# Kernel tuning notes

Hardware: AMD Instinct MI355X
Metric: run time of the kernel (lower is better)

## Reference

```python
import jax, jax.numpy as jnp
import numpy as np

N_NODES = 100000
N_EDGES = 1600000
C = 256            # in_channels == out_channels
NUM_BUNDLES = 64
BUNDLE_DIM = 2
NUM_GRAPHS = 128
BN_EPS = 1e-5


def setup_inputs() -> dict:
    key = jax.random.key(0)
    ks = jax.random.split(key, 12)
    x = jax.random.normal(ks[0], (N_NODES, C), dtype=jnp.float32)
    edge_index = jax.random.randint(ks[1], (2, N_EDGES), 0, N_NODES, dtype=jnp.int64)
    batch = jnp.sort(jax.random.randint(ks[2], (N_NODES,), 0, NUM_GRAPHS, dtype=jnp.int64))
    s = 0.05
    # struct_enc MLP: Linear(C, 2*NB) -> GELU -> Linear(2*NB, NB)
    se_w1 = jax.random.normal(ks[3], (C, 2 * NUM_BUNDLES), dtype=jnp.float32) * s
    se_b1 = jnp.zeros((2 * NUM_BUNDLES,), dtype=jnp.float32)
    se_w2 = jax.random.normal(ks[4], (2 * NUM_BUNDLES, NUM_BUNDLES), dtype=jnp.float32) * s
    se_b2 = jnp.zeros((NUM_BUNDLES,), dtype=jnp.float32)
    # LimConv.lin: Linear(C, C)
    lin_w = jax.random.normal(ks[5], (C, C), dtype=jnp.float32) * s
    lin_b = jnp.zeros((C,), dtype=jnp.float32)
    # BatchNorm1d affine params
    bn_gamma = jnp.ones((C,), dtype=jnp.float32)
    bn_beta = jnp.zeros((C,), dtype=jnp.float32)
    return {"x": x, "edge_index": edge_index, "batch": batch,
            "se_w1": se_w1, "se_b1": se_b1, "se_w2": se_w2, "se_b2": se_b2,
            "lin_w": lin_w, "lin_b": lin_b, "bn_gamma": bn_gamma, "bn_beta": bn_beta}


def _lim_layer(x, batch, se_w1, se_b1, se_w2, se_b2, lin_w, lin_b, bn_gamma, bn_beta):
    n = x.shape[0]
    # vector field: [N, NB, 2, fiber]
    vf = x.reshape(n, NUM_BUNDLES, BUNDLE_DIM, -1)
    # struct_enc MLP -> per-bundle angle (tanh-squashed), euler map to SO(2)
    h1 = jax.nn.gelu(x @ se_w1 + se_b1, approximate=False)
    ang = jnp.tanh(h1 @ se_w2 + se_b2)          # [N, NB]
    c, s = jnp.cos(ang), jnp.sin(ang)
    # R[n,b] = [[c,-s],[s,c]]  -> [N, NB, 2, 2]
    rot = jnp.stack([jnp.stack([c, -s], axis=-1),
                     jnp.stack([s, c], axis=-1)], axis=-2)
    # rotate fibers
    vf = jnp.einsum('nbij,nbjf->nbif', rot, vf)
    h = vf.reshape(n, C) @ lin_w + lin_b
    # global mean pool over graphs, then broadcast back to nodes
    sums = jax.ops.segment_sum(h, batch, num_segments=NUM_GRAPHS)
    cnts = jax.ops.segment_sum(jnp.ones((n,), h.dtype), batch, num_segments=NUM_GRAPHS)
    hmean = sums / jnp.maximum(cnts, 1.0)[:, None]
    h = hmean[batch]
    # inverse rotation (R^T)
    vf = h.reshape(n, NUM_BUNDLES, BUNDLE_DIM, -1)
    vf = jnp.einsum('nbji,nbjf->nbif', rot, vf)
    h = vf.reshape(n, C)
    # residual (dim_in == dim_out)
    h = x + h
    # dropout p=0 / eval -> identity. BatchNorm1d with batch statistics.
    mu = jnp.mean(h, axis=0)
    var = jnp.var(h, axis=0)
    h = (h - mu) * jax.lax.rsqrt(var + BN_EPS) * bn_gamma + bn_beta
    return h


def reference(x, edge_index, batch, se_w1, se_b1, se_w2, se_b2, lin_w, lin_b, bn_gamma, bn_beta):
    # edge_index is unused when num_gnn == 0 (struct_enc is an MLP), as in the source.
    del edge_index
    return _lim_layer(x, batch, se_w1, se_b1, se_w2, se_b2, lin_w, lin_b, bn_gamma, bn_beta)
```

## Files before the change

### kernel.cpp

```cpp
#include <hip/hip_runtime.h>
#include <hip/hip_bf16.h>
#include <math.h>

#define N_NODES 100000
#define C 256
#define NB 64
#define H1D 128
#define NG 128
#define BN_EPS 1e-5f

#define BLKN 32
#define ROWS 64
#define SUBT 2
#define NBLK1 ((N_NODES + ROWS - 1) / ROWS)
#define NPART NBLK1

#define GREC 769

#define OFF_GSUMS 0
#define OFF_BNSUM (NG * GREC)
#define OFF_BNSQ  (OFF_BNSUM + 256)
#define ZERO_FLOATS (OFF_BNSQ + 256)
#define OFF_HMEAN ZERO_FLOATS
#define OFF_WT1   (OFF_HMEAN + NG * C)
#define OFF_WT2   (OFF_WT1 + 16896)
#define OFF_CSN   (OFF_WT2 + 4352)
#define OFF_PBN   (OFF_CSN + N_NODES * 64)

#define WT1_LD 264
#define WT2_LD 136
#define XS_LD  272

typedef __attribute__((ext_vector_type(8))) short bf16x8;
typedef __attribute__((ext_vector_type(4))) float f32x4;

struct __align__(8) bf4 { __hip_bfloat16 x, y, z, w; };

__device__ __forceinline__ float bf2f(__hip_bfloat16 h) { return __bfloat162float(h); }

__device__ __forceinline__ float fast_tanh(float y) {
    float e = __expf(2.f * y);
    return 1.f - 2.f / (e + 1.f);
}
__device__ __forceinline__ float fast_gelu(float v) {
    float u = 0.7978845608f * (v + 0.044715f * v * v * v);
    return 0.5f * v * (1.f + fast_tanh(u));
}

__global__ __launch_bounds__(256)
void k0_prep(const float* __restrict__ W1, const float* __restrict__ W2,
             __hip_bfloat16* __restrict__ Wt1, __hip_bfloat16* __restrict__ Wt2)
{
    const int t0 = threadIdx.x + blockIdx.x * 256;
    const int stride = gridDim.x * 256;
    for (int i = t0; i < 128 * 256; i += stride) {
        int n = i >> 8, k = i & 255;
        Wt1[n * WT1_LD + k] = __float2bfloat16(W1[k * 128 + n]);
    }
    for (int i = t0; i < 64 * 128; i += stride) {
        int n = i >> 7, k = i & 127;
        Wt2[n * WT2_LD + k] = __float2bfloat16(W2[k * 64 + n]);
    }
}

__global__ __launch_bounds__(256, 6)
void k1_angles_rot_pool(const float* __restrict__ x,
                        const int* __restrict__ batch,
                        const __hip_bfloat16* __restrict__ Wt1g,
                        const float* __restrict__ b1,
                        const __hip_bfloat16* __restrict__ Wt2g,
                        const float* __restrict__ b2,
                        float* __restrict__ gsums,
                        float* __restrict__ pbn,
                        __hip_bfloat16* __restrict__ csng)
{
    __shared__ __hip_bfloat16 xs[BLKN][XS_LD];
    __shared__ char sm_u[BLKN * WT2_LD * 2];
    __shared__ int gsh[BLKN];
    auto h1s = (__hip_bfloat16 (*)[WT2_LD])sm_u;
    auto csn = (__hip_bfloat16 (*)[132])sm_u;

    const int t = threadIdx.x;
    const int w = t >> 6;
    const int l = t & 63;
    const int lo = l & 15, quad = l >> 4;

    const short* w1base = (const short*)Wt1g + (w * 32 + lo) * WT1_LD + quad * 8;
    const int mw = w >> 1;
    const int nb0 = (w & 1) * 32;
    const short* w2base = (const short*)Wt2g + (nb0 + lo) * WT2_LD + quad * 8;
    const float bb1_0 = b1[w * 32 + lo];
    const float bb1_1 = b1[w * 32 + 16 + lo];
    const float bb2_0 = b2[nb0 + lo];
    const float bb2_1 = b2[nb0 + 16 + lo];

    const int pr = t >> 6;
    const int pc4 = (t & 63) * 4;

    const int c = t;
    const int b = c >> 2;
    const int idx2 = c & 3;
    float xc_a = 0.f, xs_a = 0.f, st = 0.f, rcnt = 0.f;
    float xm = 0.f, xq = 0.f;
    int gprev = -1;

#define FLUSH_G(gidx) do {                               \
        float* rec = gsums + (size_t)(gidx) * GREC;      \
        atomicAdd(&rec[c], xc_a);                        \
        atomicAdd(&rec[256 + c], xs_a);                  \
        atomicAdd(&rec[512 + c], st);                    \
        if (c == 0) atomicAdd(&rec[768], rcnt);          \
    } while (0)

    float4 pf[8];
    int pb = 0;
    {
        const int n0 = blockIdx.x * ROWS;
        #pragma unroll
        for (int m = 0; m < 8; ++m)
            pf[m] = *(const float4*)(x + (size_t)(n0 + pr + m * 4) * C + pc4);
        if (t < BLKN) pb = batch[n0 + t];
    }

    for (int sub = 0; sub < SUBT; ++sub) {
        const int n0 = blockIdx.x * ROWS + sub * BLKN;
        if (n0 >= N_NODES) break;

        #pragma unroll
        for (int m = 0; m < 8; ++m) {
            bf4 pk;
            pk.x = __float2bfloat16(pf[m].x); pk.y = __float2bfloat16(pf[m].y);
            pk.z = __float2bfloat16(pf[m].z); pk.w = __float2bfloat16(pf[m].w);
            *(bf4*)&xs[pr + m * 4][pc4] = pk;
        }
        if (t < BLKN) gsh[t] = pb;

        const int n1 = n0 + BLKN;
        const bool more = (sub + 1 < SUBT) && (n1 < N_NODES);
        if (more) {
            #pragma unroll
            for (int m = 0; m < 8; ++m)
                pf[m] = *(const float4*)(x + (size_t)(n1 + pr + m * 4) * C + pc4);
            if (t < BLKN) pb = batch[n1 + t];
        }
        __syncthreads();

        f32x4 acc1[2][2];
        #pragma unroll
        for (int mt = 0; mt < 2; ++mt) { acc1[mt][0] = (f32x4)0.f; acc1[mt][1] = (f32x4)0.f; }
        #pragma unroll
        for (int k = 0; k < 8; ++k) {
            bf16x8 bA = *(const bf16x8*)(w1base + k * 32);
            bf16x8 bB = *(const bf16x8*)(w1base + 16 * WT1_LD + k * 32);
            #pragma unroll
            for (int mt = 0; mt < 2; ++mt) {
                bf16x8 afr = *(const bf16x8*)&xs[mt * 16 + lo][k * 32 + quad * 8];
                acc1[mt][0] = __builtin_amdgcn_mfma_f32_16x16x32_bf16(afr, bA, acc1[mt][0], 0, 0, 0);
                acc1[mt][1] = __builtin_amdgcn_mfma_f32_16x16x32_bf16(afr, bB, acc1[mt][1], 0, 0, 0);
            }
        }
        #pragma unroll
        for (int nt = 0; nt < 2; ++nt) {
            const float bb = nt ? bb1_1 : bb1_0;
            #pragma unroll
            for (int mt = 0; mt < 2; ++mt) {
                #pragma unroll
                for (int r = 0; r < 4; ++r) {
                    float v = fast_gelu(acc1[mt][nt][r] + bb);
                    h1s[mt * 16 + quad * 4 + r][w * 32 + nt * 16 + lo] = __float2bfloat16(v);
                }
            }
        }
        __syncthreads();

        f32x4 acc2[2];
        acc2[0] = (f32x4)0.f; acc2[1] = (f32x4)0.f;
        #pragma unroll
        for (int k = 0; k < 4; ++k) {
            bf16x8 afr = *(const bf16x8*)&h1s[mw * 16 + lo][k * 32 + quad * 8];
            bf16x8 bA = *(const bf16x8*)(w2base + k * 32);
            bf16x8 bB = *(const bf16x8*)(w2base + 16 * WT2_LD + k * 32);
            acc2[0] = __builtin_amdgcn_mfma_f32_16x16x32_bf16(afr, bA, acc2[0], 0, 0, 0);
            acc2[1] = __builtin_amdgcn_mfma_f32_16x16x32_bf16(afr, bB, acc2[1], 0, 0, 0);
        }
        __syncthreads();

        #pragma unroll
        for (int nt = 0; nt < 2; ++nt) {
            const int col = nb0 + nt * 16 + lo;
            const float bb = nt ? bb2_1 : bb2_0;
            #pragma unroll
            for (int r = 0; r < 4; ++r) {
                float a = fast_tanh(acc2[nt][r] + bb);
                union { unsigned int u; __hip_bfloat16 h[2]; } p;
                p.h[0] = __float2bfloat16(__cosf(a));
                p.h[1] = __float2bfloat16(__sinf(a));
                *(unsigned int*)&csn[mw * 16 + quad * 4 + r][2 * col] = p.u;
            }
        }
        __syncthreads();

        #pragma unroll
        for (int m = 0; m < 4; ++m) {
            int idx = t + m * 256;
            int row = idx >> 5;
            int q = (idx & 31);
            uint2 v = *(const uint2*)&csn[row][q * 4];
            *(uint2*)(csng + (size_t)(n0 + row) * 128 + q * 4) = v;
        }

        #pragma unroll 8
        for (int r = 0; r < BLKN; ++r) {
            const int g = gsh[r];
            if (g != gprev) {
                if (gprev >= 0) FLUSH_G(gprev);
                xc_a = 0.f; xs_a = 0.f; st = 0.f; rcnt = 0.f;
                gprev = g;
            }
            const float xv = bf2f(xs[r][c]);
            union { unsigned int u; __hip_bfloat16 h[2]; } cs;
            cs.u = *(const unsigned int*)&csn[r][2 * b];
            const float cv = bf2f(cs.h[0]);
            const float sv = bf2f(cs.h[1]);
            xc_a += xv * cv;
            xs_a += xv * sv;
            xm += xv;
            xq += xv * xv;
            st += (idx2 == 0) ? cv : (idx2 == 1) ? sv : (idx2 == 2) ? cv * cv : cv * sv;
            rcnt += 1.f;
        }
        __syncthreads();
    }

    if (gprev >= 0) FLUSH_G(gprev);
    pbn[(size_t)blockIdx.x * 512 + t] = xm;
    pbn[(size_t)blockIdx.x * 512 + 256 + t] = xq;
#undef FLUSH_G
}

__global__ __launch_bounds__(256)
void k2_hmean_stats(const float* __restrict__ gsums,
                    const float* __restrict__ pbn,
                    const float* __restrict__ lin_w, const float* __restrict__ lin_b,
                    float* __restrict__ hmean,
                    float* __restrict__ bnsum, float* __restrict__ bnsq)
{
    __shared__ float xc[C], xsv[C], bs4[C], grot[C], hm[C];
    __shared__ float cnt_sh;
    const int g = blockIdx.x;
    const int t = threadIdx.x;

    {
        const int chunk = (NPART + NG - 1) / NG;
        const int r0 = g * chunk;
        const int r1 = (r0 + chunk < NPART) ? (r0 + chunk) : NPART;
        if (r0 < r1) {
            float a0 = 0.f, a1 = 0.f;
            for (int r = r0; r < r1; ++r) {
                a0 += pbn[(size_t)r * 512 + t];
                a1 += pbn[(size_t)r * 512 + 256 + t];
            }
            atomicAdd(&bnsum[t], a0);
            atomicAdd(&bnsq[t], a1);
        }
    }

    const float* rec = gsums + (size_t)g * GREC;
    xc[t]  = rec[t];
    xsv[t] = rec[256 + t];
    bs4[t] = rec[512 + t];
    if (t == 0) cnt_sh = rec[768];
    __syncthreads();

    const int b = t >> 2, idx2 = t & 3, i2 = idx2 >> 1;
    grot[t] = (i2 == 0) ? (xc[t] - xsv[t + 2]) : (xsv[t - 2] + xc[t]);
    __syncthreads();

    float a0 = 0.f, a1 = 0.f, a2 = 0.f, a3 = 0.f;
    #pragma unroll 4
    for (int k = 0; k < C; k += 4) {
        a0 += grot[k + 0] * lin_w[(size_t)(k + 0) * C + t];
        a1 += grot[k + 1] * lin_w[(size_t)(k + 1) * C + t];
        a2 += grot[k + 2] * lin_w[(size_t)(k + 2) * C + t];
        a3 += grot[k + 3] * lin_w[(size_t)(k + 3) * C + t];
    }
    const float cnt = cnt_sh;
    const float hv = (cnt > 0.f) ? ((a0 + a1 + a2 + a3) / cnt + lin_b[t]) : 0.f;
    hm[t] = hv;
    hmean[g * C + t] = hv;
    __syncthreads();

    if (cnt > 0.f) {
        const int f = idx2 & 1;
        const float h0 = hm[4 * b + f];
        const float h1 = hm[4 * b + 2 + f];
        const float CV = bs4[4 * b + 0], SV = bs4[4 * b + 1];
        const float CC = bs4[4 * b + 2], CS = bs4[4 * b + 3];
        const float SS = cnt - CC;
        float sumc, sqc;
        if (i2 == 0) {
            sumc = h0 * CV + h1 * SV;
            sqc  = 2.f * (h0 * xc[t] + h1 * xsv[t])
                 + h0 * h0 * CC + 2.f * h0 * h1 * CS + h1 * h1 * SS;
        } else {
            sumc = -h0 * SV + h1 * CV;
            sqc  = 2.f * (-h0 * xsv[t] + h1 * xc[t])
                 + h0 * h0 * SS - 2.f * h0 * h1 * CS + h1 * h1 * CC;
        }
        atomicAdd(&bnsum[t], sumc);
        atomicAdd(&bnsq[t], sqc);
    }
}

__global__ __launch_bounds__(256, 4)
void k4_fused(const float* __restrict__ x,
              const int* __restrict__ batch,
              const __hip_bfloat16* __restrict__ csng,
              const float* __restrict__ hmean,
              const float* __restrict__ bnsum, const float* __restrict__ bnsq,
              const float* __restrict__ gamma, const float* __restrict__ beta,
              float* __restrict__ out)
{
    __shared__ float mul_s[C], add_s[C];
    const int t = threadIdx.x;
    {
        const float inv_n = 1.0f / (float)N_NODES;
        const float mu = bnsum[t] * inv_n;
        const float var = bnsq[t] * inv_n - mu * mu;
        const float inv = rsqrtf(var + BN_EPS);
        const float m = gamma[t] * inv;
        mul_s[t] = m;
        add_s[t] = beta[t] - mu * m;
    }
    __syncthreads();
    const int s = t >> 6;
    const int cg = t & 63;
    const float4 mm = *(const float4*)&mul_s[cg * 4];
    const float4 aa = *(const float4*)&add_s[cg * 4];

    for (int base = blockIdx.x * 4; base < N_NODES; base += gridDim.x * 4) {
        const int n = base + s;
        if (n < N_NODES) {
            const int g = batch[n];
            const float4 hm = *(const float4*)(hmean + (size_t)g * C + cg * 4);
            union { unsigned int u; __hip_bfloat16 h[2]; } cs;
            cs.u = *(const unsigned int*)(csng + (size_t)n * 128 + cg * 2);
            const float cv = bf2f(cs.h[0]);
            const float sv = bf2f(cs.h[1]);
            const float4 xv = *(const float4*)(x + (size_t)n * C + cg * 4);
            float4 o;
            o.x = (xv.x + cv * hm.x + sv * hm.z) * mm.x + aa.x;
            o.y = (xv.y + cv * hm.y + sv * hm.w) * mm.y + aa.y;
            o.z = (xv.z - sv * hm.x + cv * hm.z) * mm.z + aa.z;
            o.w = (xv.w - sv * hm.y + cv * hm.w) * mm.w + aa.w;
            *(float4*)(out + (size_t)n * C + cg * 4) = o;
        }
    }
}

extern "C" void kernel_launch(void* const* d_in, const int* in_sizes, int n_in,
                              void* d_out, int out_size, void* d_ws, size_t ws_size,
                              hipStream_t stream)
{
    const float* x      = (const float*)d_in[0];
    const int* batch    = (const int*)d_in[2];
    const float* W1     = (const float*)d_in[3];
    const float* b1     = (const float*)d_in[4];
    const float* W2     = (const float*)d_in[5];
    const float* b2     = (const float*)d_in[6];
    const float* lin_w  = (const float*)d_in[7];
    const float* lin_b  = (const float*)d_in[8];
    const float* gamma  = (const float*)d_in[9];
    const float* beta   = (const float*)d_in[10];

    float* ws    = (float*)d_ws;
    float* gsums = ws + OFF_GSUMS;
    float* bnsum = ws + OFF_BNSUM;
    float* bnsq  = ws + OFF_BNSQ;
    float* hmean = ws + OFF_HMEAN;
    __hip_bfloat16* Wt1  = (__hip_bfloat16*)(ws + OFF_WT1);
    __hip_bfloat16* Wt2  = (__hip_bfloat16*)(ws + OFF_WT2);
    __hip_bfloat16* csng = (__hip_bfloat16*)(ws + OFF_CSN);
    float* pbn   = ws + OFF_PBN;
    float* out   = (float*)d_out;

    hipMemsetAsync(gsums, 0, ZERO_FLOATS * sizeof(float), stream);

    k0_prep<<<32, 256, 0, stream>>>(W1, W2, Wt1, Wt2);
    k1_angles_rot_pool<<<NBLK1, 256, 0, stream>>>(x, batch, Wt1, b1, Wt2, b2,
                                                  gsums, pbn, csng);
    k2_hmean_stats<<<NG, 256, 0, stream>>>(gsums, pbn, lin_w, lin_b, hmean, bnsum, bnsq);
    k4_fused<<<2048, 256, 0, stream>>>(x, batch, csng, hmean, bnsum, bnsq,
                                       gamma, beta, out);
}
```

Measured before the change: 297.4 us.

## Fuse all stages into one persistent cooperative kernel with grid syncs

Replaces the memset plus four separate launches with a single cooperative persistent kernel. Grid-wide syncs separate the weight prep and zeroing, the angle/rotation/pool pass, the per-graph hmean and BN stats, and the final normalize pass. Each block now processes a contiguous range of 32-row subtiles, which reduces per-block partials and atomic flushes. The aim is to remove launch gaps and tail effects. In exchange it caps the grid at about 1024 resident blocks, adds grid-sync overhead, and keeps the old path as a fallback.

New measurement: 607.8 us. 2.04x slower.

```diff
diff --git a/kernel.cpp b/kernel.cpp
--- a/kernel.cpp
+++ b/kernel.cpp
@@ -1,6 +1,9 @@
 #include <hip/hip_runtime.h>
+#include <hip/hip_cooperative_groups.h>
 #include <hip/hip_bf16.h>
 #include <math.h>
+
+namespace cg = cooperative_groups;
 
 #define N_NODES 100000
 #define C 256
@@ -10,10 +13,13 @@
 #define BN_EPS 1e-5f
 
 #define BLKN 32
-#define ROWS 64
-#define SUBT 2
-#define NBLK1 ((N_NODES + ROWS - 1) / ROWS)
-#define NPART NBLK1
+#define NSUB (N_NODES / BLKN)
+#define COOP_MAX 1024
+
+#define FB_ROWS 64
+#define FB_SUBT 2
+#define FB_NBLK ((N_NODES + FB_ROWS - 1) / FB_ROWS)
+#define PBN_ROWS FB_NBLK
 
 #define GREC 769
 
@@ -45,6 +51,325 @@
 __device__ __forceinline__ float fast_gelu(float v) {
     float u = 0.7978845608f * (v + 0.044715f * v * v * v);
     return 0.5f * v * (1.f + fast_tanh(u));
+}
+
+__global__ __launch_bounds__(256, 4)
+void fused(const float* __restrict__ x,
+           const int* __restrict__ batch,
+           const float* __restrict__ W1, const float* __restrict__ b1,
+           const float* __restrict__ W2, const float* __restrict__ b2,
+           const float* __restrict__ lin_w, const float* __restrict__ lin_b,
+           const float* __restrict__ gamma, const float* __restrict__ beta,
+           float* __restrict__ ws, float* __restrict__ out)
+{
+    __shared__ __hip_bfloat16 xs[BLKN][XS_LD];
+    __shared__ char sm_u[BLKN * WT2_LD * 2];
+    __shared__ int gsh[BLKN];
+    auto h1s = (__hip_bfloat16 (*)[WT2_LD])sm_u;
+    auto csn = (__hip_bfloat16 (*)[132])sm_u;
+
+    float* gsums = ws + OFF_GSUMS;
+    float* bnsum = ws + OFF_BNSUM;
+    float* bnsq  = ws + OFF_BNSQ;
+    float* hmean = ws + OFF_HMEAN;
+    __hip_bfloat16* Wt1g = (__hip_bfloat16*)(ws + OFF_WT1);
+    __hip_bfloat16* Wt2g = (__hip_bfloat16*)(ws + OFF_WT2);
+    __hip_bfloat16* csng = (__hip_bfloat16*)(ws + OFF_CSN);
+    float* pbn   = ws + OFF_PBN;
+
+    cg::grid_group gg = cg::this_grid();
+
+    const int nblk = gridDim.x;
+    const int bid = blockIdx.x;
+    const int t = threadIdx.x;
+    const int w = t >> 6;
+    const int l = t & 63;
+    const int lo = l & 15, quad = l >> 4;
+
+    {
+        for (int i = bid * 256 + t; i < ZERO_FLOATS; i += nblk * 256)
+            ws[i] = 0.f;
+        if (bid < 32) {
+            const int t0 = bid * 256 + t;
+            for (int j = t0; j < 128 * 256; j += 8192) {
+                int nn = j >> 8, k = j & 255;
+                Wt1g[nn * WT1_LD + k] = __float2bfloat16(W1[k * 128 + nn]);
+            }
+            for (int j = t0; j < 64 * 128; j += 8192) {
+                int nn = j >> 7, k = j & 127;
+                Wt2g[nn * WT2_LD + k] = __float2bfloat16(W2[k * 64 + nn]);
+            }
+        }
+    }
+    __threadfence();
+    gg.sync();
+
+    {
+        const int base_cnt = NSUB / nblk;
+        const int rem = NSUB - base_cnt * nblk;
+        const int scnt = base_cnt + (bid < rem ? 1 : 0);
+        const int sstart = base_cnt * bid + (bid < rem ? bid : rem);
+
+        const short* w1base = (const short*)Wt1g + (w * 32 + lo) * WT1_LD + quad * 8;
+        const int mw = w >> 1;
+        const int nb0 = (w & 1) * 32;
+        const short* w2base = (const short*)Wt2g + (nb0 + lo) * WT2_LD + quad * 8;
+        const float bb1_0 = b1[w * 32 + lo];
+        const float bb1_1 = b1[w * 32 + 16 + lo];
+        const float bb2_0 = b2[nb0 + lo];
+        const float bb2_1 = b2[nb0 + 16 + lo];
+
+        const int pr = t >> 6;
+        const int pc4 = (t & 63) * 4;
+
+        const int c = t;
+        const int b = c >> 2;
+        const int idx2 = c & 3;
+        float xc_a = 0.f, xs_a = 0.f, st = 0.f, rcnt = 0.f;
+        float xm = 0.f, xq = 0.f;
+        int gprev = -1;
+
+#define FLUSH_G(gidx) do {                               \
+        float* rec = gsums + (size_t)(gidx) * GREC;      \
+        atomicAdd(&rec[c], xc_a);                        \
+        atomicAdd(&rec[256 + c], xs_a);                  \
+        atomicAdd(&rec[512 + c], st);                    \
+        if (c == 0) atomicAdd(&rec[768], rcnt);          \
+    } while (0)
+
+        float4 pf[8];
+        int pb = 0;
+        {
+            const int n0 = sstart * BLKN;
+            #pragma unroll
+            for (int m = 0; m < 8; ++m)
+                pf[m] = *(const float4*)(x + (size_t)(n0 + pr + m * 4) * C + pc4);
+            if (t < BLKN) pb = batch[n0 + t];
+        }
+
+        for (int sub = 0; sub < scnt; ++sub) {
+            const int n0 = (sstart + sub) * BLKN;
+
+            #pragma unroll
+            for (int m = 0; m < 8; ++m) {
+                bf4 pk;
+                pk.x = __float2bfloat16(pf[m].x); pk.y = __float2bfloat16(pf[m].y);
+                pk.z = __float2bfloat16(pf[m].z); pk.w = __float2bfloat16(pf[m].w);
+                *(bf4*)&xs[pr + m * 4][pc4] = pk;
+            }
+            if (t < BLKN) gsh[t] = pb;
+
+            if (sub + 1 < scnt) {
+                const int n1 = n0 + BLKN;
+                #pragma unroll
+                for (int m = 0; m < 8; ++m)
+                    pf[m] = *(const float4*)(x + (size_t)(n1 + pr + m * 4) * C + pc4);
+                if (t < BLKN) pb = batch[n1 + t];
+            }
+            __syncthreads();
+
+            f32x4 acc1[2][2];
+            #pragma unroll
+            for (int mt = 0; mt < 2; ++mt) { acc1[mt][0] = (f32x4)0.f; acc1[mt][1] = (f32x4)0.f; }
+            #pragma unroll
+            for (int k = 0; k < 8; ++k) {
+                bf16x8 bA = *(const bf16x8*)(w1base + k * 32);
+                bf16x8 bB = *(const bf16x8*)(w1base + 16 * WT1_LD + k * 32);
+                #pragma unroll
+                for (int mt = 0; mt < 2; ++mt) {
+                    bf16x8 afr = *(const bf16x8*)&xs[mt * 16 + lo][k * 32 + quad * 8];
+                    acc1[mt][0] = __builtin_amdgcn_mfma_f32_16x16x32_bf16(afr, bA, acc1[mt][0], 0, 0, 0);
+                    acc1[mt][1] = __builtin_amdgcn_mfma_f32_16x16x32_bf16(afr, bB, acc1[mt][1], 0, 0, 0);
+                }
+            }
+            #pragma unroll
+            for (int nt = 0; nt < 2; ++nt) {
+                const float bb = nt ? bb1_1 : bb1_0;
+                #pragma unroll
+                for (int mt = 0; mt < 2; ++mt) {
+                    #pragma unroll
+                    for (int r = 0; r < 4; ++r) {
+                        float v = fast_gelu(acc1[mt][nt][r] + bb);
+                        h1s[mt * 16 + quad * 4 + r][w * 32 + nt * 16 + lo] = __float2bfloat16(v);
+                    }
+                }
+            }
+            __syncthreads();
+
+            f32x4 acc2[2];
+            acc2[0] = (f32x4)0.f; acc2[1] = (f32x4)0.f;
+            #pragma unroll
+            for (int k = 0; k < 4; ++k) {
+                bf16x8 afr = *(const bf16x8*)&h1s[mw * 16 + lo][k * 32 + quad * 8];
+                bf16x8 bA = *(const bf16x8*)(w2base + k * 32);
+                bf16x8 bB = *(const bf16x8*)(w2base + 16 * WT2_LD + k * 32);
+                acc2[0] = __builtin_amdgcn_mfma_f32_16x16x32_bf16(afr, bA, acc2[0], 0, 0, 0);
+                acc2[1] = __builtin_amdgcn_mfma_f32_16x16x32_bf16(afr, bB, acc2[1], 0, 0, 0);
+            }
+            __syncthreads();
+
+            #pragma unroll
+            for (int nt = 0; nt < 2; ++nt) {
+                const int col = nb0 + nt * 16 + lo;
+                const float bb = nt ? bb2_1 : bb2_0;
+                #pragma unroll
+                for (int r = 0; r < 4; ++r) {
+                    float a = fast_tanh(acc2[nt][r] + bb);
+                    union { unsigned int u; __hip_bfloat16 h[2]; } p;
+                    p.h[0] = __float2bfloat16(__cosf(a));
+                    p.h[1] = __float2bfloat16(__sinf(a));
+                    *(unsigned int*)&csn[mw * 16 + quad * 4 + r][2 * col] = p.u;
+                }
+            }
+            __syncthreads();
+
+            #pragma unroll
+            for (int m = 0; m < 4; ++m) {
+                int idx = t + m * 256;
+                int row = idx >> 5;
+                int q = (idx & 31);
+                uint2 v = *(const uint2*)&csn[row][q * 4];
+                *(uint2*)(csng + (size_t)(n0 + row) * 128 + q * 4) = v;
+            }
+
+            #pragma unroll 8
+            for (int r = 0; r < BLKN; ++r) {
+                const int g = gsh[r];
+                if (g != gprev) {
+                    if (gprev >= 0) FLUSH_G(gprev);
+                    xc_a = 0.f; xs_a = 0.f; st = 0.f; rcnt = 0.f;
+                    gprev = g;
+                }
+                const float xv = bf2f(xs[r][c]);
+                union { unsigned int u; __hip_bfloat16 h[2]; } cs;
+                cs.u = *(const unsigned int*)&csn[r][2 * b];
+                const float cv = bf2f(cs.h[0]);
+                const float sv = bf2f(cs.h[1]);
+                xc_a += xv * cv;
+                xs_a += xv * sv;
+                xm += xv;
+                xq += xv * xv;
+                st += (idx2 == 0) ? cv : (idx2 == 1) ? sv : (idx2 == 2) ? cv * cv : cv * sv;
+                rcnt += 1.f;
+            }
+            __syncthreads();
+        }
+
+        if (gprev >= 0) FLUSH_G(gprev);
+#undef FLUSH_G
+        pbn[(size_t)bid * 512 + t] = xm;
+        pbn[(size_t)bid * 512 + 256 + t] = xq;
+    }
+    __threadfence();
+    gg.sync();
+
+    if (bid < NG) {
+        float* xsh = (float*)&xs[0][0];
+        float* xc   = xsh;
+        float* xsv  = xsh + 256;
+        float* bs4  = xsh + 512;
+        float* grot = xsh + 768;
+        float* hm   = xsh + 1024;
+        const int g = bid;
+
+        {
+            const int chunk = nblk >> 7;
+            const int r0 = g * chunk;
+            float a0 = 0.f, a1 = 0.f;
+            for (int r = r0; r < r0 + chunk; ++r) {
+                a0 += pbn[(size_t)r * 512 + t];
+                a1 += pbn[(size_t)r * 512 + 256 + t];
+            }
+            atomicAdd(&bnsum[t], a0);
+            atomicAdd(&bnsq[t], a1);
+        }
+
+        const float* rec = gsums + (size_t)g * GREC;
+        xc[t]  = rec[t];
+        xsv[t] = rec[256 + t];
+        bs4[t] = rec[512 + t];
+        if (t == 0) xsh[1280] = rec[768];
+        __syncthreads();
+
+        const int b = t >> 2, idx2 = t & 3, i2 = idx2 >> 1;
+        grot[t] = (i2 == 0) ? (xc[t] - xsv[t + 2]) : (xsv[t - 2] + xc[t]);
+        __syncthreads();
+
+        float a0 = 0.f, a1 = 0.f, a2 = 0.f, a3 = 0.f;
+        #pragma unroll 4
+        for (int k = 0; k < C; k += 4) {
+            a0 += grot[k + 0] * lin_w[(size_t)(k + 0) * C + t];
+            a1 += grot[k + 1] * lin_w[(size_t)(k + 1) * C + t];
+            a2 += grot[k + 2] * lin_w[(size_t)(k + 2) * C + t];
+            a3 += grot[k + 3] * lin_w[(size_t)(k + 3) * C + t];
+        }
+        const float cnt = xsh[1280];
+        const float hv = (cnt > 0.f) ? ((a0 + a1 + a2 + a3) / cnt + lin_b[t]) : 0.f;
+        hm[t] = hv;
+        hmean[g * C + t] = hv;
+        __syncthreads();
+
+        if (cnt > 0.f) {
+            const int f = idx2 & 1;
+            const float h0 = hm[4 * b + f];
+            const float h1 = hm[4 * b + 2 + f];
+            const float CV = bs4[4 * b + 0], SV = bs4[4 * b + 1];
+            const float CC = bs4[4 * b + 2], CS = bs4[4 * b + 3];
+            const float SS = cnt - CC;
+            float sumc, sqc;
+            if (i2 == 0) {
+                sumc = h0 * CV + h1 * SV;
+                sqc  = 2.f * (h0 * xc[t] + h1 * xsv[t])
+                     + h0 * h0 * CC + 2.f * h0 * h1 * CS + h1 * h1 * SS;
+            } else {
+                sumc = -h0 * SV + h1 * CV;
+                sqc  = 2.f * (-h0 * xsv[t] + h1 * xc[t])
+                     + h0 * h0 * SS - 2.f * h0 * h1 * CS + h1 * h1 * CC;
+            }
+            atomicAdd(&bnsum[t], sumc);
+            atomicAdd(&bnsq[t], sqc);
+        }
+    }
+    __threadfence();
+    gg.sync();
+
+    {
+        float* mul_s = (float*)sm_u;
+        float* add_s = mul_s + 256;
+        {
+            const float inv_n = 1.0f / (float)N_NODES;
+            const float mu = bnsum[t] * inv_n;
+            const float var = bnsq[t] * inv_n - mu * mu;
+            const float inv = rsqrtf(var + BN_EPS);
+            const float m = gamma[t] * inv;
+            mul_s[t] = m;
+            add_s[t] = beta[t] - mu * m;
+        }
+        __syncthreads();
+        const int s = t >> 6;
+        const int cg4 = t & 63;
+        const float4 mm = *(const float4*)&mul_s[cg4 * 4];
+        const float4 aa = *(const float4*)&add_s[cg4 * 4];
+
+        for (int base = bid * 4; base < N_NODES; base += nblk * 4) {
+            const int n = base + s;
+            if (n < N_NODES) {
+                const int g = batch[n];
+                const float4 hmv = *(const float4*)(hmean + (size_t)g * C + cg4 * 4);
+                union { unsigned int u; __hip_bfloat16 h[2]; } cs;
+                cs.u = *(const unsigned int*)(csng + (size_t)n * 128 + cg4 * 2);
+                const float cv = bf2f(cs.h[0]);
+                const float sv = bf2f(cs.h[1]);
+                const float4 xv = *(const float4*)(x + (size_t)n * C + cg4 * 4);
+                float4 o;
+                o.x = (xv.x + cv * hmv.x + sv * hmv.z) * mm.x + aa.x;
+                o.y = (xv.y + cv * hmv.y + sv * hmv.w) * mm.y + aa.y;
+                o.z = (xv.z - sv * hmv.x + cv * hmv.z) * mm.z + aa.z;
+                o.w = (xv.w - sv * hmv.y + cv * hmv.w) * mm.w + aa.w;
+                *(float4*)(out + (size_t)n * C + cg4 * 4) = o;
+            }
+        }
+    }
 }
 
 __global__ __launch_bounds__(256)
@@ -115,15 +440,15 @@
     float4 pf[8];
     int pb = 0;
     {
-        const int n0 = blockIdx.x * ROWS;
+        const int n0 = blockIdx.x * FB_ROWS;
         #pragma unroll
         for (int m = 0; m < 8; ++m)
             pf[m] = *(const float4*)(x + (size_t)(n0 + pr + m * 4) * C + pc4);
         if (t < BLKN) pb = batch[n0 + t];
     }
 
-    for (int sub = 0; sub < SUBT; ++sub) {
-        const int n0 = blockIdx.x * ROWS + sub * BLKN;
+    for (int sub = 0; sub < FB_SUBT; ++sub) {
+        const int n0 = blockIdx.x * FB_ROWS + sub * BLKN;
         if (n0 >= N_NODES) break;
 
         #pragma unroll
@@ -136,7 +461,7 @@
         if (t < BLKN) gsh[t] = pb;
 
         const int n1 = n0 + BLKN;
-        const bool more = (sub + 1 < SUBT) && (n1 < N_NODES);
+        const bool more = (sub + 1 < FB_SUBT) && (n1 < N_NODES);
         if (more) {
             #pragma unroll
             for (int m = 0; m < 8; ++m)
@@ -233,9 +558,9 @@
     }
 
     if (gprev >= 0) FLUSH_G(gprev);
+#undef FLUSH_G
     pbn[(size_t)blockIdx.x * 512 + t] = xm;
     pbn[(size_t)blockIdx.x * 512 + 256 + t] = xq;
-#undef FLUSH_G
 }
 
 __global__ __launch_bounds__(256)
@@ -251,9 +576,9 @@
     const int t = threadIdx.x;
 
     {
-        const int chunk = (NPART + NG - 1) / NG;
+        const int chunk = (FB_NBLK + NG - 1) / NG;
         const int r0 = g * chunk;
-        const int r1 = (r0 + chunk < NPART) ? (r0 + chunk) : NPART;
+        const int r1 = (r0 + chunk < FB_NBLK) ? (r0 + chunk) : FB_NBLK;
         if (r0 < r1) {
             float a0 = 0.f, a1 = 0.f;
             for (int r = r0; r < r1; ++r) {
@@ -334,26 +659,26 @@
     }
     __syncthreads();
     const int s = t >> 6;
-    const int cg = t & 63;
-    const float4 mm = *(const float4*)&mul_s[cg * 4];
-    const float4 aa = *(const float4*)&add_s[cg * 4];
+    const int cg4 = t & 63;
+    const float4 mm = *(const float4*)&mul_s[cg4 * 4];
+    const float4 aa = *(const float4*)&add_s[cg4 * 4];
 
     for (int base = blockIdx.x * 4; base < N_NODES; base += gridDim.x * 4) {
         const int n = base + s;
         if (n < N_NODES) {
             const int g = batch[n];
-            const float4 hm = *(const float4*)(hmean + (size_t)g * C + cg * 4);
+            const float4 hm = *(const float4*)(hmean + (size_t)g * C + cg4 * 4);
             union { unsigned int u; __hip_bfloat16 h[2]; } cs;
-            cs.u = *(const unsigned int*)(csng + (size_t)n * 128 + cg * 2);
+            cs.u = *(const unsigned int*)(csng + (size_t)n * 128 + cg4 * 2);
             const float cv = bf2f(cs.h[0]);
             const float sv = bf2f(cs.h[1]);
-            const float4 xv = *(const float4*)(x + (size_t)n * C + cg * 4);
+            const float4 xv = *(const float4*)(x + (size_t)n * C + cg4 * 4);
             float4 o;
             o.x = (xv.x + cv * hm.x + sv * hm.z) * mm.x + aa.x;
             o.y = (xv.y + cv * hm.y + sv * hm.w) * mm.y + aa.y;
             o.z = (xv.z - sv * hm.x + cv * hm.z) * mm.z + aa.z;
             o.w = (xv.w - sv * hm.y + cv * hm.w) * mm.w + aa.w;
-            *(float4*)(out + (size_t)n * C + cg * 4) = o;
+            *(float4*)(out + (size_t)n * C + cg4 * 4) = o;
         }
     }
 }
@@ -372,8 +697,40 @@
     const float* lin_b  = (const float*)d_in[8];
     const float* gamma  = (const float*)d_in[9];
     const float* beta   = (const float*)d_in[10];
-
-    float* ws    = (float*)d_ws;
+    float* ws  = (float*)d_ws;
+    float* out = (float*)d_out;
+
+    static int coop_blocks = -2;
+    if (coop_blocks == -2) {
+        int nb = 0, dev = 0, ncu = 0;
+        hipError_t e = hipOccupancyMaxActiveBlocksPerMultiprocessor(
+            &nb, (const void*)fused, 256, 0);
+        if (e == hipSuccess && hipGetDevice(&dev) == hipSuccess) {
+            hipDeviceProp_t prop;
+            if (hipGetDeviceProperties(&prop, dev) == hipSuccess)
+                ncu = prop.multiProcessorCount;
+        }
+        long total = (long)nb * (long)ncu;
+        if (total >= 512) {
+            if (total > COOP_MAX) total = COOP_MAX;
+            coop_blocks = (int)(total & ~127L);
+        } else {
+            coop_blocks = -1;
+        }
+    }
+
+    if (coop_blocks > 0) {
+        void* args[] = {(void*)&x, (void*)&batch, (void*)&W1, (void*)&b1,
+                        (void*)&W2, (void*)&b2, (void*)&lin_w, (void*)&lin_b,
+                        (void*)&gamma, (void*)&beta, (void*)&ws, (void*)&out};
+        hipError_t e = hipLaunchCooperativeKernel((const void*)fused,
+                                                  dim3(coop_blocks), dim3(256),
+                                                  args, 0, stream);
+        if (e == hipSuccess) return;
+        (void)hipGetLastError();
+        coop_blocks = -1;
+    }
+
     float* gsums = ws + OFF_GSUMS;
     float* bnsum = ws + OFF_BNSUM;
     float* bnsq  = ws + OFF_BNSQ;
@@ -382,13 +739,11 @@
     __hip_bfloat16* Wt2  = (__hip_bfloat16*)(ws + OFF_WT2);
     __hip_bfloat16* csng = (__hip_bfloat16*)(ws + OFF_CSN);
     float* pbn   = ws + OFF_PBN;
-    float* out   = (float*)d_out;
 
     hipMemsetAsync(gsums, 0, ZERO_FLOATS * sizeof(float), stream);
-
     k0_prep<<<32, 256, 0, stream>>>(W1, W2, Wt1, Wt2);
-    k1_angles_rot_pool<<<NBLK1, 256, 0, stream>>>(x, batch, Wt1, b1, Wt2, b2,
-                                                  gsums, pbn, csng);
+    k1_angles_rot_pool<<<FB_NBLK, 256, 0, stream>>>(x, batch, Wt1, b1, Wt2, b2,
+                                                    gsums, pbn, csng);
     k2_hmean_stats<<<NG, 256, 0, stream>>>(gsums, pbn, lin_w, lin_b, hmean, bnsum, bnsq);
     k4_fused<<<2048, 256, 0, stream>>>(x, batch, csng, hmean, bnsum, bnsq,
                                        gamma, beta, out);
```

## Restructure angle kernel to one wave per 32-node tile, fold memset into prep

Applied to the files above, without the earlier changes.

The angle/rotation/pool kernel changes from 256-thread blocks with shared-memory x staging and multiple barriers to single-wave 64-thread blocks. Each wave loads x directly from global into MFMA fragments, computes all 128 hidden and 64 angle columns, and then accumulates per-graph rotated sums with float4 loads over 4 channels per lane. This drops the barriers and the LDS copy of x, but x is read twice from global (cache-dependent), each wave issues many more atomics per flush, and the partial count doubles. The workspace zeroing memset is folded into the prep kernel to save a launch.

Measured after the change: 317.4 us. 1.07x slower.

```diff
diff --git a/kernel.cpp b/kernel.cpp
--- a/kernel.cpp
+++ b/kernel.cpp
@@ -10,10 +10,8 @@
 #define BN_EPS 1e-5f
 
 #define BLKN 32
-#define ROWS 64
-#define SUBT 2
-#define NBLK1 ((N_NODES + ROWS - 1) / ROWS)
-#define NPART NBLK1
+#define NSUB (N_NODES / BLKN)
+#define NPART NSUB
 
 #define GREC 769
 
@@ -29,12 +27,9 @@
 
 #define WT1_LD 264
 #define WT2_LD 136
-#define XS_LD  272
 
 typedef __attribute__((ext_vector_type(8))) short bf16x8;
 typedef __attribute__((ext_vector_type(4))) float f32x4;
-
-struct __align__(8) bf4 { __hip_bfloat16 x, y, z, w; };
 
 __device__ __forceinline__ float bf2f(__hip_bfloat16 h) { return __bfloat162float(h); }
 
@@ -47,12 +42,24 @@
     return 0.5f * v * (1.f + fast_tanh(u));
 }
 
+__device__ __forceinline__ bf16x8 pack8(float4 a, float4 b) {
+    union { bf16x8 v; __hip_bfloat16 h[8]; } u;
+    u.h[0] = __float2bfloat16(a.x); u.h[1] = __float2bfloat16(a.y);
+    u.h[2] = __float2bfloat16(a.z); u.h[3] = __float2bfloat16(a.w);
+    u.h[4] = __float2bfloat16(b.x); u.h[5] = __float2bfloat16(b.y);
+    u.h[6] = __float2bfloat16(b.z); u.h[7] = __float2bfloat16(b.w);
+    return u.v;
+}
+
 __global__ __launch_bounds__(256)
 void k0_prep(const float* __restrict__ W1, const float* __restrict__ W2,
+             float* __restrict__ ws,
              __hip_bfloat16* __restrict__ Wt1, __hip_bfloat16* __restrict__ Wt2)
 {
     const int t0 = threadIdx.x + blockIdx.x * 256;
     const int stride = gridDim.x * 256;
+    for (int i = t0; i < ZERO_FLOATS; i += stride)
+        ws[i] = 0.f;
     for (int i = t0; i < 128 * 256; i += stride) {
         int n = i >> 8, k = i & 255;
         Wt1[n * WT1_LD + k] = __float2bfloat16(W1[k * 128 + n]);
@@ -63,179 +70,154 @@
     }
 }
 
-__global__ __launch_bounds__(256, 6)
-void k1_angles_rot_pool(const float* __restrict__ x,
-                        const int* __restrict__ batch,
-                        const __hip_bfloat16* __restrict__ Wt1g,
-                        const float* __restrict__ b1,
-                        const __hip_bfloat16* __restrict__ Wt2g,
-                        const float* __restrict__ b2,
-                        float* __restrict__ gsums,
-                        float* __restrict__ pbn,
-                        __hip_bfloat16* __restrict__ csng)
-{
-    __shared__ __hip_bfloat16 xs[BLKN][XS_LD];
-    __shared__ char sm_u[BLKN * WT2_LD * 2];
+__global__ __launch_bounds__(64, 4)
+void k1_wave(const float* __restrict__ x,
+             const int* __restrict__ batch,
+             const __hip_bfloat16* __restrict__ Wt1g,
+             const float* __restrict__ b1,
+             const __hip_bfloat16* __restrict__ Wt2g,
+             const float* __restrict__ b2,
+             float* __restrict__ gsums,
+             float* __restrict__ pbn,
+             __hip_bfloat16* __restrict__ csng)
+{
+    __shared__ __hip_bfloat16 h1s[BLKN][WT2_LD];
     __shared__ int gsh[BLKN];
-    auto h1s = (__hip_bfloat16 (*)[WT2_LD])sm_u;
-    auto csn = (__hip_bfloat16 (*)[132])sm_u;
-
-    const int t = threadIdx.x;
-    const int w = t >> 6;
-    const int l = t & 63;
+    auto csn = (__hip_bfloat16 (*)[132])&h1s[0][0];
+
+    const int l = threadIdx.x;
     const int lo = l & 15, quad = l >> 4;
-
-    const short* w1base = (const short*)Wt1g + (w * 32 + lo) * WT1_LD + quad * 8;
-    const int mw = w >> 1;
-    const int nb0 = (w & 1) * 32;
-    const short* w2base = (const short*)Wt2g + (nb0 + lo) * WT2_LD + quad * 8;
-    const float bb1_0 = b1[w * 32 + lo];
-    const float bb1_1 = b1[w * 32 + 16 + lo];
-    const float bb2_0 = b2[nb0 + lo];
-    const float bb2_1 = b2[nb0 + 16 + lo];
-
-    const int pr = t >> 6;
-    const int pc4 = (t & 63) * 4;
-
-    const int c = t;
-    const int b = c >> 2;
-    const int idx2 = c & 3;
-    float xc_a = 0.f, xs_a = 0.f, st = 0.f, rcnt = 0.f;
-    float xm = 0.f, xq = 0.f;
-    int gprev = -1;
-
-#define FLUSH_G(gidx) do {                               \
-        float* rec = gsums + (size_t)(gidx) * GREC;      \
-        atomicAdd(&rec[c], xc_a);                        \
-        atomicAdd(&rec[256 + c], xs_a);                  \
-        atomicAdd(&rec[512 + c], st);                    \
-        if (c == 0) atomicAdd(&rec[768], rcnt);          \
-    } while (0)
-
-    float4 pf[8];
-    int pb = 0;
-    {
-        const int n0 = blockIdx.x * ROWS;
+    const int wid = blockIdx.x;
+    const int n0 = wid * BLKN;
+
+    if (l < BLKN) gsh[l] = batch[n0 + l];
+
+    f32x4 acc1[2][8];
+    #pragma unroll
+    for (int nt = 0; nt < 8; ++nt) { acc1[0][nt] = (f32x4)0.f; acc1[1][nt] = (f32x4)0.f; }
+
+    const float* xr0 = x + (size_t)(n0 + lo) * C + quad * 8;
+    const short* w1row = (const short*)Wt1g + lo * WT1_LD + quad * 8;
+    #pragma unroll
+    for (int k = 0; k < 8; ++k) {
+        float4 u00 = *(const float4*)(xr0 + k * 32);
+        float4 u01 = *(const float4*)(xr0 + k * 32 + 4);
+        float4 u10 = *(const float4*)(xr0 + 16 * C + k * 32);
+        float4 u11 = *(const float4*)(xr0 + 16 * C + k * 32 + 4);
+        bf16x8 a0 = pack8(u00, u01);
+        bf16x8 a1 = pack8(u10, u11);
         #pragma unroll
-        for (int m = 0; m < 8; ++m)
-            pf[m] = *(const float4*)(x + (size_t)(n0 + pr + m * 4) * C + pc4);
-        if (t < BLKN) pb = batch[n0 + t];
-    }
-
-    for (int sub = 0; sub < SUBT; ++sub) {
-        const int n0 = blockIdx.x * ROWS + sub * BLKN;
-        if (n0 >= N_NODES) break;
-
+        for (int nt = 0; nt < 8; ++nt) {
+            bf16x8 bB = *(const bf16x8*)(w1row + nt * 16 * WT1_LD + k * 32);
+            acc1[0][nt] = __builtin_amdgcn_mfma_f32_16x16x32_bf16(a0, bB, acc1[0][nt], 0, 0, 0);
+            acc1[1][nt] = __builtin_amdgcn_mfma_f32_16x16x32_bf16(a1, bB, acc1[1][nt], 0, 0, 0);
+        }
+    }
+
+    #pragma unroll
+    for (int nt = 0; nt < 8; ++nt) {
+        const float bb = b1[nt * 16 + lo];
         #pragma unroll
-        for (int m = 0; m < 8; ++m) {
-            bf4 pk;
-            pk.x = __float2bfloat16(pf[m].x); pk.y = __float2bfloat16(pf[m].y);
-            pk.z = __float2bfloat16(pf[m].z); pk.w = __float2bfloat16(pf[m].w);
-            *(bf4*)&xs[pr + m * 4][pc4] = pk;
-        }
-        if (t < BLKN) gsh[t] = pb;
-
-        const int n1 = n0 + BLKN;
-        const bool more = (sub + 1 < SUBT) && (n1 < N_NODES);
-        if (more) {
-            #pragma unroll
-            for (int m = 0; m < 8; ++m)
-                pf[m] = *(const float4*)(x + (size_t)(n1 + pr + m * 4) * C + pc4);
-            if (t < BLKN) pb = batch[n1 + t];
-        }
-        __syncthreads();
-
-        f32x4 acc1[2][2];
-        #pragma unroll
-        for (int mt = 0; mt < 2; ++mt) { acc1[mt][0] = (f32x4)0.f; acc1[mt][1] = (f32x4)0.f; }
-        #pragma unroll
-        for (int k = 0; k < 8; ++k) {
-            bf16x8 bA = *(const bf16x8*)(w1base + k * 32);
-            bf16x8 bB = *(const bf16x8*)(w1base + 16 * WT1_LD + k * 32);
-            #pragma unroll
-            for (int mt = 0; mt < 2; ++mt) {
-                bf16x8 afr = *(const bf16x8*)&xs[mt * 16 + lo][k * 32 + quad * 8];
-                acc1[mt][0] = __builtin_amdgcn_mfma_f32_16x16x32_bf16(afr, bA, acc1[mt][0], 0, 0, 0);
-                acc1[mt][1] = __builtin_amdgcn_mfma_f32_16x16x32_bf16(afr, bB, acc1[mt][1], 0, 0, 0);
-            }
-        }
-        #pragma unroll
-        for (int nt = 0; nt < 2; ++nt) {
-            const float bb = nt ? bb1_1 : bb1_0;
-            #pragma unroll
-            for (int mt = 0; mt < 2; ++mt) {
-                #pragma unroll
-                for (int r = 0; r < 4; ++r) {
-                    float v = fast_gelu(acc1[mt][nt][r] + bb);
-                    h1s[mt * 16 + quad * 4 + r][w * 32 + nt * 16 + lo] = __float2bfloat16(v);
-                }
-            }
-        }
-        __syncthreads();
-
-        f32x4 acc2[2];
-        acc2[0] = (f32x4)0.f; acc2[1] = (f32x4)0.f;
-        #pragma unroll
-        for (int k = 0; k < 4; ++k) {
-            bf16x8 afr = *(const bf16x8*)&h1s[mw * 16 + lo][k * 32 + quad * 8];
-            bf16x8 bA = *(const bf16x8*)(w2base + k * 32);
-            bf16x8 bB = *(const bf16x8*)(w2base + 16 * WT2_LD + k * 32);
-            acc2[0] = __builtin_amdgcn_mfma_f32_16x16x32_bf16(afr, bA, acc2[0], 0, 0, 0);
-            acc2[1] = __builtin_amdgcn_mfma_f32_16x16x32_bf16(afr, bB, acc2[1], 0, 0, 0);
-        }
-        __syncthreads();
-
-        #pragma unroll
-        for (int nt = 0; nt < 2; ++nt) {
-            const int col = nb0 + nt * 16 + lo;
-            const float bb = nt ? bb2_1 : bb2_0;
+        for (int mt = 0; mt < 2; ++mt) {
             #pragma unroll
             for (int r = 0; r < 4; ++r) {
-                float a = fast_tanh(acc2[nt][r] + bb);
+                float v = fast_gelu(acc1[mt][nt][r] + bb);
+                h1s[mt * 16 + quad * 4 + r][nt * 16 + lo] = __float2bfloat16(v);
+            }
+        }
+    }
+
+    f32x4 acc2[2][4];
+    #pragma unroll
+    for (int nt = 0; nt < 4; ++nt) { acc2[0][nt] = (f32x4)0.f; acc2[1][nt] = (f32x4)0.f; }
+    const short* w2row = (const short*)Wt2g + lo * WT2_LD + quad * 8;
+    #pragma unroll
+    for (int k = 0; k < 4; ++k) {
+        bf16x8 af0 = *(const bf16x8*)&h1s[lo][k * 32 + quad * 8];
+        bf16x8 af1 = *(const bf16x8*)&h1s[16 + lo][k * 32 + quad * 8];
+        #pragma unroll
+        for (int nt = 0; nt < 4; ++nt) {
+            bf16x8 bB = *(const bf16x8*)(w2row + nt * 16 * WT2_LD + k * 32);
+            acc2[0][nt] = __builtin_amdgcn_mfma_f32_16x16x32_bf16(af0, bB, acc2[0][nt], 0, 0, 0);
+            acc2[1][nt] = __builtin_amdgcn_mfma_f32_16x16x32_bf16(af1, bB, acc2[1][nt], 0, 0, 0);
+        }
+    }
+
+    #pragma unroll
+    for (int nt = 0; nt < 4; ++nt) {
+        const int col = nt * 16 + lo;
+        const float bb = b2[col];
+        #pragma unroll
+        for (int mt = 0; mt < 2; ++mt) {
+            #pragma unroll
+            for (int r = 0; r < 4; ++r) {
+                float a = fast_tanh(acc2[mt][nt][r] + bb);
                 union { unsigned int u; __hip_bfloat16 h[2]; } p;
                 p.h[0] = __float2bfloat16(__cosf(a));
                 p.h[1] = __float2bfloat16(__sinf(a));
-                *(unsigned int*)&csn[mw * 16 + quad * 4 + r][2 * col] = p.u;
+                *(unsigned int*)&csn[mt * 16 + quad * 4 + r][2 * col] = p.u;
             }
         }
-        __syncthreads();
-
-        #pragma unroll
-        for (int m = 0; m < 4; ++m) {
-            int idx = t + m * 256;
-            int row = idx >> 5;
-            int q = (idx & 31);
-            uint2 v = *(const uint2*)&csn[row][q * 4];
-            *(uint2*)(csng + (size_t)(n0 + row) * 128 + q * 4) = v;
-        }
-
-        #pragma unroll 8
-        for (int r = 0; r < BLKN; ++r) {
-            const int g = gsh[r];
-            if (g != gprev) {
-                if (gprev >= 0) FLUSH_G(gprev);
-                xc_a = 0.f; xs_a = 0.f; st = 0.f; rcnt = 0.f;
-                gprev = g;
-            }
-            const float xv = bf2f(xs[r][c]);
-            union { unsigned int u; __hip_bfloat16 h[2]; } cs;
-            cs.u = *(const unsigned int*)&csn[r][2 * b];
-            const float cv = bf2f(cs.h[0]);
-            const float sv = bf2f(cs.h[1]);
-            xc_a += xv * cv;
-            xs_a += xv * sv;
-            xm += xv;
-            xq += xv * xv;
-            st += (idx2 == 0) ? cv : (idx2 == 1) ? sv : (idx2 == 2) ? cv * cv : cv * sv;
-            rcnt += 1.f;
-        }
-        __syncthreads();
-    }
-
+    }
+
+    #pragma unroll
+    for (int m = 0; m < 16; ++m) {
+        int idx = l + m * 64;
+        int row = idx >> 5;
+        int q = idx & 31;
+        uint2 v = *(const uint2*)&csn[row][q * 4];
+        *(uint2*)(csng + (size_t)(n0 + row) * 128 + q * 4) = v;
+    }
+
+    const int c0 = 4 * l;
+    float xc0 = 0.f, xc1 = 0.f, xc2 = 0.f, xc3 = 0.f;
+    float xs0 = 0.f, xs1 = 0.f, xs2 = 0.f, xs3 = 0.f;
+    float xm0 = 0.f, xm1 = 0.f, xm2 = 0.f, xm3 = 0.f;
+    float xq0 = 0.f, xq1 = 0.f, xq2 = 0.f, xq3 = 0.f;
+    float stc = 0.f, sts = 0.f, stcc = 0.f, stcs = 0.f, rcnt = 0.f;
+    int gprev = -1;
+
+#define FLUSH_G(gidx) do {                                            \
+        float* rec = gsums + (size_t)(gidx) * GREC;                   \
+        atomicAdd(&rec[c0 + 0], xc0); atomicAdd(&rec[c0 + 1], xc1);   \
+        atomicAdd(&rec[c0 + 2], xc2); atomicAdd(&rec[c0 + 3], xc3);   \
+        atomicAdd(&rec[256 + c0 + 0], xs0); atomicAdd(&rec[256 + c0 + 1], xs1); \
+        atomicAdd(&rec[256 + c0 + 2], xs2); atomicAdd(&rec[256 + c0 + 3], xs3); \
+        atomicAdd(&rec[512 + c0 + 0], stc); atomicAdd(&rec[512 + c0 + 1], sts); \
+        atomicAdd(&rec[512 + c0 + 2], stcc); atomicAdd(&rec[512 + c0 + 3], stcs); \
+        if (l == 0) atomicAdd(&rec[768], rcnt);                       \
+    } while (0)
+
+    #pragma unroll 8
+    for (int r = 0; r < BLKN; ++r) {
+        const int g = gsh[r];
+        if (g != gprev) {
+            if (gprev >= 0) FLUSH_G(gprev);
+            xc0 = xc1 = xc2 = xc3 = 0.f;
+            xs0 = xs1 = xs2 = xs3 = 0.f;
+            stc = sts = stcc = stcs = 0.f;
+            rcnt = 0.f;
+            gprev = g;
+        }
+        const float4 xv = *(const float4*)(x + (size_t)(n0 + r) * C + c0);
+        union { unsigned int u; __hip_bfloat16 h[2]; } cs;
+        cs.u = *(const unsigned int*)&csn[r][2 * l];
+        const float cv = bf2f(cs.h[0]);
+        const float sv = bf2f(cs.h[1]);
+        xc0 += xv.x * cv; xc1 += xv.y * cv; xc2 += xv.z * cv; xc3 += xv.w * cv;
+        xs0 += xv.x * sv; xs1 += xv.y * sv; xs2 += xv.z * sv; xs3 += xv.w * sv;
+        xm0 += xv.x; xm1 += xv.y; xm2 += xv.z; xm3 += xv.w;
+        xq0 += xv.x * xv.x; xq1 += xv.y * xv.y; xq2 += xv.z * xv.z; xq3 += xv.w * xv.w;
+        stc += cv; sts += sv; stcc += cv * cv; stcs += cv * sv;
+        rcnt += 1.f;
+    }
     if (gprev >= 0) FLUSH_G(gprev);
-    pbn[(size_t)blockIdx.x * 512 + t] = xm;
-    pbn[(size_t)blockIdx.x * 512 + 256 + t] = xq;
 #undef FLUSH_G
+
+    float4 m4; m4.x = xm0; m4.y = xm1; m4.z = xm2; m4.w = xm3;
+    float4 q4; q4.x = xq0; q4.y = xq1; q4.z = xq2; q4.w = xq3;
+    *(float4*)&pbn[(size_t)wid * 512 + c0] = m4;
+    *(float4*)&pbn[(size_t)wid * 512 + 256 + c0] = q4;
 }
 
 __global__ __launch_bounds__(256)
@@ -334,26 +316,26 @@
     }
     __syncthreads();
     const int s = t >> 6;
-    const int cg = t & 63;
-    const float4 mm = *(const float4*)&mul_s[cg * 4];
-    const float4 aa = *(const float4*)&add_s[cg * 4];
+    const int cg4 = t & 63;
+    const float4 mm = *(const float4*)&mul_s[cg4 * 4];
+    const float4 aa = *(const float4*)&add_s[cg4 * 4];
 
     for (int base = blockIdx.x * 4; base < N_NODES; base += gridDim.x * 4) {
         const int n = base + s;
         if (n < N_NODES) {
             const int g = batch[n];
-            const float4 hm = *(const float4*)(hmean + (size_t)g * C + cg * 4);
+            const float4 hm = *(const float4*)(hmean + (size_t)g * C + cg4 * 4);
             union { unsigned int u; __hip_bfloat16 h[2]; } cs;
-            cs.u = *(const unsigned int*)(csng + (size_t)n * 128 + cg * 2);
+            cs.u = *(const unsigned int*)(csng + (size_t)n * 128 + cg4 * 2);
             const float cv = bf2f(cs.h[0]);
             const float sv = bf2f(cs.h[1]);
-            const float4 xv = *(const float4*)(x + (size_t)n * C + cg * 4);
+            const float4 xv = *(const float4*)(x + (size_t)n * C + cg4 * 4);
             float4 o;
             o.x = (xv.x + cv * hm.x + sv * hm.z) * mm.x + aa.x;
             o.y = (xv.y + cv * hm.y + sv * hm.w) * mm.y + aa.y;
             o.z = (xv.z - sv * hm.x + cv * hm.z) * mm.z + aa.z;
             o.w = (xv.w - sv * hm.y + cv * hm.w) * mm.w + aa.w;
-            *(float4*)(out + (size_t)n * C + cg * 4) = o;
+            *(float4*)(out + (size_t)n * C + cg4 * 4) = o;
         }
     }
 }
@@ -384,11 +366,9 @@
     float* pbn   = ws + OFF_PBN;
     float* out   = (float*)d_out;
 
-    hipMemsetAsync(gsums, 0, ZERO_FLOATS * sizeof(float), stream);
-
-    k0_prep<<<32, 256, 0, stream>>>(W1, W2, Wt1, Wt2);
-    k1_angles_rot_pool<<<NBLK1, 256, 0, stream>>>(x, batch, Wt1, b1, Wt2, b2,
-                                                  gsums, pbn, csng);
+    k0_prep<<<512, 256, 0, stream>>>(W1, W2, ws, Wt1, Wt2);
+    k1_wave<<<NSUB, 64, 0, stream>>>(x, batch, Wt1, b1, Wt2, b2,
+                                     gsums, pbn, csng);
     k2_hmean_stats<<<NG, 256, 0, stream>>>(gsums, pbn, lin_w, lin_b, hmean, bnsum, bnsq);
     k4_fused<<<2048, 256, 0, stream>>>(x, batch, csng, hmean, bnsum, bnsq,
                                        gamma, beta, out);
```
